# Performance work log

Measured on AMD Instinct MI355X. Metric: run time of the kernel, lower is better.

The kernel has to match this reference:

```python
import jax, jax.numpy as jnp
import numpy as np

BITS = 4
MAXQ = 15            # 2**BITS - 1
PACK = 32 // BITS    # 8 int4 values per int32
GROUPSIZE = 128
M, K, N = 2048, 4096, 4096
G = K // GROUPSIZE


def setup_inputs() -> dict:
    key = jax.random.key(0)
    k1, k2, k3, k4, k5 = jax.random.split(key, 5)
    x = jax.random.normal(k1, (M, K), dtype=jnp.float32)
    qweight = jax.random.randint(k2, (K // PACK, N), 0, 2147483647, dtype=jnp.int32)
    qzeros = jax.random.randint(k3, (G, N // PACK), 0, 2147483647, dtype=jnp.int32)
    scales = jax.random.uniform(k4, (G, N), dtype=jnp.float32) * 0.01
    g_idx = (jnp.arange(K, dtype=jnp.int32) // GROUPSIZE).astype(jnp.int32)
    bias = jax.random.normal(k5, (N,), dtype=jnp.float32)
    return {"x": x, "qweight": qweight, "qzeros": qzeros,
            "scales": scales, "g_idx": g_idx, "bias": bias}


def _dequantize(qweight, qzeros, scales, g_idx):
    shifts = (jnp.arange(PACK, dtype=jnp.int32) * BITS)
    # unpack weights along K: [K//8, N] -> [K//8, 8, N] -> [K, N]
    w_int = ((qweight[:, None, :] >> shifts[None, :, None]) & MAXQ)
    w_int = w_int.reshape(K, N)
    # unpack zeros along N: [G, N//8] -> [G, N//8, 8] -> [G, N]; kernel adds 1
    z_int = ((qzeros[:, :, None] >> shifts[None, None, :]) & MAXQ) + 1
    z_int = z_int.reshape(G, N)
    # group-wise dequant: W[k, n] = (w - zeros[g_idx[k]]) * scales[g_idx[k]]
    W = (w_int - z_int[g_idx]).astype(jnp.float32) * scales[g_idx]
    return W  # [K, N]


def reference(x, qweight, qzeros, scales, g_idx, bias):
    W = _dequantize(qweight, qzeros, scales, g_idx)
    return x @ W + bias  # [M, N]
```

## Files before the change

### kernel.cpp

```cpp
#include <hip/hip_runtime.h>
#include <hip/hip_bf16.h>
#include <stdint.h>

#define M_DIM 2048
#define K_DIM 4096
#define N_DIM 4096

typedef __attribute__((ext_vector_type(8))) short short8;
typedef __attribute__((ext_vector_type(4))) float f32x4;

#define MFMA __builtin_amdgcn_mfma_f32_16x16x32_bf16

__device__ __forceinline__ uint32_t bf16pk(float a, float b) {
  uint32_t ua = __float_as_uint(a);
  ua = (ua + 0x7FFFu + ((ua >> 16) & 1u)) >> 16;
  uint32_t ub = __float_as_uint(b);
  ub = (ub + 0x7FFFu + ((ub >> 16) & 1u)) >> 16;
  return ua | (ub << 16);
}

__device__ __forceinline__ void glds16(const char* g, char* l) {
  __builtin_amdgcn_global_load_lds((__attribute__((address_space(1))) void*)g,
                                   (__attribute__((address_space(3))) void*)l, 16, 0, 0);
}


__global__ void __launch_bounds__(256) prep_kernel(const float* __restrict__ x,
                                                   const uint32_t* __restrict__ qweight,
                                                   const uint32_t* __restrict__ qzeros,
                                                   const float* __restrict__ scales,
                                                   char* __restrict__ xImg,
                                                   char* __restrict__ wImg) {
  const int tid = threadIdx.x;
  if (blockIdx.x < 1024) {
    const int bid = blockIdx.x;
    const int mt = bid >> 6, ktp = bid & 63;
    const int row = tid & 127, sh = tid >> 7;
    const int s = ktp * 2 + sh;
    const float* src = x + (size_t)(mt * 128 + row) * K_DIM + s * 32;
    char* dst = xImg + (size_t)(mt * 128 + s) * 8192 + row * 16;
#pragma unroll
    for (int slot = 0; slot < 4; ++slot) {
      float4 f0 = *(const float4*)(src + slot * 8);
      float4 f1 = *(const float4*)(src + slot * 8 + 4);
      uint4 pk;
      pk.x = bf16pk(f0.x, f0.y);
      pk.y = bf16pk(f0.z, f0.w);
      pk.z = bf16pk(f1.x, f1.y);
      pk.w = bf16pk(f1.z, f1.w);
      *(uint4*)(dst + slot * 2048) = pk;
    }
  } else {
    const int bid = blockIdx.x - 1024;
    const int nt = bid >> 6, ktp = bid & 63;
    const int n = tid & 127, sh = tid >> 7;
    const int s = ktp * 2 + sh;
    const int g = ktp >> 1;
    const int gn = nt * 128 + n;
    uint32_t zq = qzeros[g * (N_DIM / 8) + (gn >> 3)];
    const int z = (int)((zq >> ((gn & 7) * 4)) & 15u) + 1;
    const float s_ = scales[g * N_DIM + gn];
    char* dst = wImg + (size_t)(nt * 128 + s) * 8192 + n * 16;
#pragma unroll
    for (int slot = 0; slot < 4; ++slot) {
      uint32_t q = qweight[(size_t)(s * 4 + slot) * N_DIM + gn];
      float f[8];
#pragma unroll
      for (int v = 0; v < 8; ++v) {
        int w = (int)((q >> (4 * v)) & 15u);
        f[v] = (float)(w - z) * s_;
      }
      uint4 pk;
      pk.x = bf16pk(f[0], f[1]);
      pk.y = bf16pk(f[2], f[3]);
      pk.z = bf16pk(f[4], f[5]);
      pk.w = bf16pk(f[6], f[7]);
      *(uint4*)(dst + slot * 2048) = pk;
    }
  }
}

__global__ void __launch_bounds__(512, 1) gemm_kernel(const char* __restrict__ xImg,
                                                      const char* __restrict__ wImg,
                                                      const float* __restrict__ bias,
                                                      float* __restrict__ out) {
  __shared__ uint4 ldsv[9216];
  char* lds = (char*)ldsv;
  const int tid = threadIdx.x;
  const int lane = tid & 63, wid = tid >> 6;
  const int ks = wid >> 2, wc = wid & 3;
  const int lr = lane & 15, lk = lane >> 4;

  const int bid = blockIdx.x;
  const int local = bid >> 3, xcd = bid & 7;
  const int nb = xcd * 2 + (local & 1);
  const int mb = local >> 1;

  f32x4 acc[8][4];
#pragma unroll
  for (int i = 0; i < 8; ++i)
#pragma unroll
    for (int j = 0; j < 4; ++j) acc[i][j] = f32x4{0.f, 0.f, 0.f, 0.f};

  const char* aT = xImg + (size_t)mb * 128 * 8192;
  const char* bT0 = wImg + (size_t)(2 * nb) * 128 * 8192;
  const char* bT1 = wImg + (size_t)(2 * nb + 1) * 128 * 8192;

  int aoff[8], boff[4];
#pragma unroll
  for (int i = 0; i < 8; ++i) aoff[i] = ks * 8192 + lk * 2048 + (i * 16 + lr) * 16;
#pragma unroll
  for (int j = 0; j < 4; ++j)
    boff[j] = 16384 + ks * 16384 + (wc >> 1) * 8192 + lk * 2048 +
              ((wc & 1) * 64 + j * 16 + lr) * 16;

#define STAGE(T, SLOT)                                                     \
  do {                                                                     \
    char* d = lds + (SLOT) * 49152;                                        \
    glds16(aT + (size_t)(T) * 8192 + tid * 16, d + tid * 16);              \
    glds16(aT + (size_t)(64 + (T)) * 8192 + tid * 16, d + 8192 + tid * 16);\
    glds16(bT0 + (size_t)(T) * 8192 + tid * 16, d + 16384 + tid * 16);     \
    glds16(bT1 + (size_t)(T) * 8192 + tid * 16, d + 24576 + tid * 16);     \
    glds16(bT0 + (size_t)(64 + (T)) * 8192 + tid * 16, d + 32768 + tid * 16);\
    glds16(bT1 + (size_t)(64 + (T)) * 8192 + tid * 16, d + 40960 + tid * 16);\
  } while (0)

  short8 vA[2][8], vB[2][4];

  STAGE(0, 0);
  asm volatile("s_waitcnt vmcnt(0)" ::: "memory");
  __builtin_amdgcn_sched_barrier(0);
  __builtin_amdgcn_s_barrier();
#pragma unroll
  for (int i = 0; i < 8; ++i) vA[0][i] = *(const short8*)(lds + aoff[i]);
#pragma unroll
  for (int j = 0; j < 4; ++j) vB[0][j] = *(const short8*)(lds + boff[j]);
  STAGE(1, 1);
  asm volatile("s_waitcnt vmcnt(0)" ::: "memory");
  __builtin_amdgcn_sched_barrier(0);
  __builtin_amdgcn_s_barrier();

#pragma unroll 2
  for (int t = 0; t < 64; ++t) {
    const int cs = t & 1, ns = cs ^ 1;

    if (t < 63) {
      const char* rbuf = lds + ((t + 1) % 3) * 49152;
#pragma unroll
      for (int i = 0; i < 8; ++i) vA[ns][i] = *(const short8*)(rbuf + aoff[i]);
#pragma unroll
      for (int j = 0; j < 4; ++j) vB[ns][j] = *(const short8*)(rbuf + boff[j]);
    }
    if (t < 62) STAGE(t + 2, (t + 2) % 3);
    __builtin_amdgcn_sched_barrier(0);

    if (t < 63) asm volatile("s_waitcnt lgkmcnt(12)" ::: "memory");
    else        asm volatile("s_waitcnt lgkmcnt(0)" ::: "memory");
    __builtin_amdgcn_sched_barrier(0);

    __builtin_amdgcn_s_setprio(1);
#pragma unroll
    for (int j = 0; j < 4; ++j) {
#pragma unroll
      for (int i = 0; i < 8; ++i)
        acc[i][j] = MFMA(vA[cs][i], vB[cs][j], acc[i][j], 0, 0, 0);
    }
    __builtin_amdgcn_s_setprio(0);

    if (t < 63) {
      asm volatile("s_waitcnt vmcnt(0)" ::: "memory");
      __builtin_amdgcn_sched_barrier(0);
      __builtin_amdgcn_s_barrier();
    }
  }
#undef STAGE

  __syncthreads();
  if (ks == 1) {
#pragma unroll
    for (int i = 0; i < 4; ++i)
#pragma unroll
      for (int j = 0; j < 4; ++j)
        *(f32x4*)(lds + (wc * 16 + i * 4 + j) * 1024 + lane * 16) = acc[i][j];
  } else {
#pragma unroll
    for (int i = 4; i < 8; ++i)
#pragma unroll
      for (int j = 0; j < 4; ++j)
        *(f32x4*)(lds + 65536 + (wc * 16 + (i - 4) * 4 + j) * 1024 + lane * 16) = acc[i][j];
  }
  __syncthreads();

  const int colB = nb * 256 + wc * 64 + lr;
  if (ks == 0) {
#pragma unroll
    for (int j = 0; j < 4; ++j) {
      int col = colB + j * 16;
      float bj = bias[col];
#pragma unroll
      for (int i = 0; i < 4; ++i) {
        f32x4 p = *(const f32x4*)(lds + (wc * 16 + i * 4 + j) * 1024 + lane * 16);
        int row = mb * 128 + i * 16 + lk * 4;
#pragma unroll
        for (int r = 0; r < 4; ++r)
          out[(size_t)(row + r) * N_DIM + col] = acc[i][j][r] + p[r] + bj;
      }
    }
  } else {
#pragma unroll
    for (int j = 0; j < 4; ++j) {
      int col = colB + j * 16;
      float bj = bias[col];
#pragma unroll
      for (int i = 4; i < 8; ++i) {
        f32x4 p = *(const f32x4*)(lds + 65536 + (wc * 16 + (i - 4) * 4 + j) * 1024 + lane * 16);
        int row = mb * 128 + i * 16 + lk * 4;
#pragma unroll
        for (int r = 0; r < 4; ++r)
          out[(size_t)(row + r) * N_DIM + col] = acc[i][j][r] + p[r] + bj;
      }
    }
  }
}

__global__ void fallback_kernel(const float* __restrict__ x, const uint32_t* __restrict__ qweight,
                                const uint32_t* __restrict__ qzeros, const float* __restrict__ scales,
                                const float* __restrict__ bias, float* __restrict__ out) {
  __shared__ float xs[16][17];
  __shared__ float ws[16][17];
  int tx = threadIdx.x, ty = threadIdx.y;
  int col = blockIdx.x * 16 + tx;
  int row = blockIdx.y * 16 + ty;
  float acc = 0.f;
  for (int k0 = 0; k0 < K_DIM; k0 += 16) {
    xs[ty][tx] = x[(size_t)row * K_DIM + k0 + tx];
    int k = k0 + ty;
    int g = k >> 7;
    uint32_t q = qweight[(size_t)(k >> 3) * N_DIM + col];
    int w = (int)((q >> ((k & 7) * 4)) & 15u);
    uint32_t zq = qzeros[g * (N_DIM / 8) + (col >> 3)];
    int z = (int)((zq >> ((col & 7) * 4)) & 15u) + 1;
    ws[ty][tx] = (float)(w - z) * scales[g * N_DIM + col];
    __syncthreads();
#pragma unroll
    for (int kk = 0; kk < 16; ++kk) acc += xs[ty][kk] * ws[kk][tx];
    __syncthreads();
  }
  out[(size_t)row * N_DIM + col] = acc + bias[col];
}

extern "C" void kernel_launch(void* const* d_in, const int* in_sizes, int n_in,
                              void* d_out, int out_size, void* d_ws, size_t ws_size,
                              hipStream_t stream) {
  const float* x = (const float*)d_in[0];
  const uint32_t* qweight = (const uint32_t*)d_in[1];
  const uint32_t* qzeros = (const uint32_t*)d_in[2];
  const float* scales = (const float*)d_in[3];
  const float* bias = (const float*)d_in[5];
  float* out = (float*)d_out;

  const size_t X_IMG = (size_t)16 * 128 * 8192;
  const size_t W_IMG = (size_t)32 * 128 * 8192;

  if (ws_size >= X_IMG + W_IMG) {
    char* xImg = (char*)d_ws;
    char* wImg = (char*)d_ws + X_IMG;
    prep_kernel<<<3072, 256, 0, stream>>>(x, qweight, qzeros, scales, xImg, wImg);
    gemm_kernel<<<256, 512, 0, stream>>>(xImg, wImg, bias, out);
  } else {
    fallback_kernel<<<dim3(N_DIM / 16, M_DIM / 16), dim3(16, 16), 0, stream>>>(
        x, qweight, qzeros, scales, bias, out);
  }
}
```

Before: 84.62 us.

## Drop split-K wave groups in GEMM, use 4 waves over full K

Workgroups shrink from 8 waves, split as two K-halves plus an LDS reduction, to 4 waves that each walk the full K range in 128 steps. Each stage still loads the same bytes per tile, but one workgroup's 4 waves now cover a whole K slab. This removes the epilogue LDS reduction and its two syncs and halves LDS use. In exchange the main loop has twice as many barrier-separated iterations, and with one 256-thread block per CU only 4 waves are resident, which reduces latency hiding.

```diff
diff --git a/kernel.cpp b/kernel.cpp
--- a/kernel.cpp
+++ b/kernel.cpp
@@ -80,19 +80,18 @@
   }
 }
 
-__global__ void __launch_bounds__(512, 1) gemm_kernel(const char* __restrict__ xImg,
+__global__ void __launch_bounds__(256, 1) gemm_kernel(const char* __restrict__ xImg,
                                                       const char* __restrict__ wImg,
                                                       const float* __restrict__ bias,
                                                       float* __restrict__ out) {
-  __shared__ uint4 ldsv[9216];
+  __shared__ uint4 ldsv[4608];
   char* lds = (char*)ldsv;
   const int tid = threadIdx.x;
-  const int lane = tid & 63, wid = tid >> 6;
-  const int ks = wid >> 2, wc = wid & 3;
+  const int lane = tid & 63, wc = tid >> 6;
   const int lr = lane & 15, lk = lane >> 4;
 
   const int bid = blockIdx.x;
-  const int local = bid >> 3, xcd = bid & 7;
+  const int xcd = bid & 7, local = bid >> 3;
   const int nb = xcd * 2 + (local & 1);
   const int mb = local >> 1;
 
@@ -108,21 +107,20 @@
 
   int aoff[8], boff[4];
 #pragma unroll
-  for (int i = 0; i < 8; ++i) aoff[i] = ks * 8192 + lk * 2048 + (i * 16 + lr) * 16;
+  for (int i = 0; i < 8; ++i) aoff[i] = lk * 2048 + (i * 16 + lr) * 16;
 #pragma unroll
   for (int j = 0; j < 4; ++j)
-    boff[j] = 16384 + ks * 16384 + (wc >> 1) * 8192 + lk * 2048 +
-              ((wc & 1) * 64 + j * 16 + lr) * 16;
-
-#define STAGE(T, SLOT)                                                     \
-  do {                                                                     \
-    char* d = lds + (SLOT) * 49152;                                        \
-    glds16(aT + (size_t)(T) * 8192 + tid * 16, d + tid * 16);              \
-    glds16(aT + (size_t)(64 + (T)) * 8192 + tid * 16, d + 8192 + tid * 16);\
-    glds16(bT0 + (size_t)(T) * 8192 + tid * 16, d + 16384 + tid * 16);     \
-    glds16(bT1 + (size_t)(T) * 8192 + tid * 16, d + 24576 + tid * 16);     \
-    glds16(bT0 + (size_t)(64 + (T)) * 8192 + tid * 16, d + 32768 + tid * 16);\
-    glds16(bT1 + (size_t)(64 + (T)) * 8192 + tid * 16, d + 40960 + tid * 16);\
+    boff[j] = 8192 + (wc >> 1) * 8192 + lk * 2048 + ((wc & 1) * 64 + j * 16 + lr) * 16;
+
+#define STAGE(T, SLOT)                                                      \
+  do {                                                                      \
+    char* d = lds + (SLOT) * 24576;                                         \
+    glds16(aT + (size_t)(T) * 8192 + tid * 16, d + tid * 16);               \
+    glds16(aT + (size_t)(T) * 8192 + 4096 + tid * 16, d + 4096 + tid * 16); \
+    glds16(bT0 + (size_t)(T) * 8192 + tid * 16, d + 8192 + tid * 16);       \
+    glds16(bT0 + (size_t)(T) * 8192 + 4096 + tid * 16, d + 12288 + tid * 16);\
+    glds16(bT1 + (size_t)(T) * 8192 + tid * 16, d + 16384 + tid * 16);      \
+    glds16(bT1 + (size_t)(T) * 8192 + 4096 + tid * 16, d + 20480 + tid * 16);\
   } while (0)
 
   short8 vA[2][8], vB[2][4];
@@ -141,21 +139,21 @@
   __builtin_amdgcn_s_barrier();
 
 #pragma unroll 2
-  for (int t = 0; t < 64; ++t) {
+  for (int t = 0; t < 128; ++t) {
     const int cs = t & 1, ns = cs ^ 1;
 
-    if (t < 63) {
-      const char* rbuf = lds + ((t + 1) % 3) * 49152;
+    if (t < 127) {
+      const char* rbuf = lds + ((t + 1) % 3) * 24576;
 #pragma unroll
       for (int i = 0; i < 8; ++i) vA[ns][i] = *(const short8*)(rbuf + aoff[i]);
 #pragma unroll
       for (int j = 0; j < 4; ++j) vB[ns][j] = *(const short8*)(rbuf + boff[j]);
     }
-    if (t < 62) STAGE(t + 2, (t + 2) % 3);
+    if (t < 126) STAGE(t + 2, (t + 2) % 3);
     __builtin_amdgcn_sched_barrier(0);
 
-    if (t < 63) asm volatile("s_waitcnt lgkmcnt(12)" ::: "memory");
-    else        asm volatile("s_waitcnt lgkmcnt(0)" ::: "memory");
+    if (t < 127) asm volatile("s_waitcnt lgkmcnt(12)" ::: "memory");
+    else         asm volatile("s_waitcnt lgkmcnt(0)" ::: "memory");
     __builtin_amdgcn_sched_barrier(0);
 
     __builtin_amdgcn_s_setprio(1);
@@ -167,7 +165,7 @@
     }
     __builtin_amdgcn_s_setprio(0);
 
-    if (t < 63) {
+    if (t < 127) {
       asm volatile("s_waitcnt vmcnt(0)" ::: "memory");
       __builtin_amdgcn_sched_barrier(0);
       __builtin_amdgcn_s_barrier();
@@ -175,50 +173,17 @@
   }
 #undef STAGE
 
-  __syncthreads();
-  if (ks == 1) {
-#pragma unroll
-    for (int i = 0; i < 4; ++i)
-#pragma unroll
-      for (int j = 0; j < 4; ++j)
-        *(f32x4*)(lds + (wc * 16 + i * 4 + j) * 1024 + lane * 16) = acc[i][j];
-  } else {
-#pragma unroll
-    for (int i = 4; i < 8; ++i)
-#pragma unroll
-      for (int j = 0; j < 4; ++j)
-        *(f32x4*)(lds + 65536 + (wc * 16 + (i - 4) * 4 + j) * 1024 + lane * 16) = acc[i][j];
-  }
-  __syncthreads();
-
   const int colB = nb * 256 + wc * 64 + lr;
-  if (ks == 0) {
-#pragma unroll
-    for (int j = 0; j < 4; ++j) {
-      int col = colB + j * 16;
-      float bj = bias[col];
-#pragma unroll
-      for (int i = 0; i < 4; ++i) {
-        f32x4 p = *(const f32x4*)(lds + (wc * 16 + i * 4 + j) * 1024 + lane * 16);
-        int row = mb * 128 + i * 16 + lk * 4;
-#pragma unroll
-        for (int r = 0; r < 4; ++r)
-          out[(size_t)(row + r) * N_DIM + col] = acc[i][j][r] + p[r] + bj;
-      }
-    }
-  } else {
-#pragma unroll
-    for (int j = 0; j < 4; ++j) {
-      int col = colB + j * 16;
-      float bj = bias[col];
-#pragma unroll
-      for (int i = 4; i < 8; ++i) {
-        f32x4 p = *(const f32x4*)(lds + 65536 + (wc * 16 + (i - 4) * 4 + j) * 1024 + lane * 16);
-        int row = mb * 128 + i * 16 + lk * 4;
-#pragma unroll
-        for (int r = 0; r < 4; ++r)
-          out[(size_t)(row + r) * N_DIM + col] = acc[i][j][r] + p[r] + bj;
-      }
+#pragma unroll
+  for (int j = 0; j < 4; ++j) {
+    int col = colB + j * 16;
+    float bj = bias[col];
+#pragma unroll
+    for (int i = 0; i < 8; ++i) {
+      int row = mb * 128 + i * 16 + lk * 4;
+#pragma unroll
+      for (int r = 0; r < 4; ++r)
+        out[(size_t)(row + r) * N_DIM + col] = acc[i][j][r] + bj;
     }
   }
 }
@@ -266,7 +231,7 @@
     char* xImg = (char*)d_ws;
     char* wImg = (char*)d_ws + X_IMG;
     prep_kernel<<<3072, 256, 0, stream>>>(x, qweight, qzeros, scales, xImg, wImg);
-    gemm_kernel<<<256, 512, 0, stream>>>(xImg, wImg, bias, out);
+    gemm_kernel<<<256, 256, 0, stream>>>(xImg, wImg, bias, out);
   } else {
     fallback_kernel<<<dim3(N_DIM / 16, M_DIM / 16), dim3(16, 16), 0, stream>>>(
         x, qweight, qzeros, scales, bias, out);
```

Result: slower. 117.0 us (+38.3%).
